# Optimization experiments

Hardware: AMD Instinct MI355X
Metric: run time of the kernel (lower is better)

## Reference

```python
import jax, jax.numpy as jnp
import numpy as np

N_HEAD = 16
HEAD_DIM = 64
ROPE_BASE = 10000.0


def _rope(t):
    # t: [B, H, C, D]; rotate-half RoPE, offset 0
    B, H, C, D = t.shape
    inv_freq = 1.0 / (ROPE_BASE ** (jnp.arange(0, D, 2, dtype=jnp.float32) / D))  # [D/2]
    ang = jnp.arange(C, dtype=jnp.float32)[:, None] * inv_freq[None, :]           # [C, D/2]
    cos = jnp.concatenate([jnp.cos(ang), jnp.cos(ang)], axis=-1)                  # [C, D]
    sin = jnp.concatenate([jnp.sin(ang), jnp.sin(ang)], axis=-1)                  # [C, D]
    t1, t2 = jnp.split(t, 2, axis=-1)
    rot = jnp.concatenate([-t2, t1], axis=-1)
    return t * cos.astype(t.dtype) + rot * sin.astype(t.dtype)


def setup_inputs() -> dict:
    key = jax.random.key(0)
    ks = jax.random.split(key, 5)
    E = 1024
    B, C = 2, 2048
    s = 1.0 / np.sqrt(E)
    return {
        "x": jax.random.normal(ks[0], (B, C, E), dtype=jnp.float32),
        "Wq": jax.random.normal(ks[1], (E, E), dtype=jnp.float32) * s,
        "Wk": jax.random.normal(ks[2], (E, E), dtype=jnp.float32) * s,
        "Wv": jax.random.normal(ks[3], (E, E), dtype=jnp.float32) * s,
        "Wo": jax.random.normal(ks[4], (E, E), dtype=jnp.float32) * s,
    }


def reference(x, Wq, Wk, Wv, Wo):
    B, C, E = x.shape
    H, D = N_HEAD, HEAD_DIM
    # nn.Linear(bias=False): y = x @ W.T
    Q = (x @ Wq.T).reshape(B, C, H, D).transpose(0, 2, 1, 3)  # [B,H,C,D]
    K = (x @ Wk.T).reshape(B, C, H, D).transpose(0, 2, 1, 3)
    V = (x @ Wv.T).reshape(B, C, H, D).transpose(0, 2, 1, 3)
    Q = _rope(Q)
    K = _rope(K)
    scores = jnp.einsum("bhqd,bhkd->bhqk", Q, K) / jnp.sqrt(jnp.float32(D))
    causal = jnp.tril(jnp.ones((C, C), dtype=bool))
    scores = jnp.where(causal, scores, jnp.float32(-jnp.inf))
    weights = jax.nn.softmax(scores, axis=-1)
    hidden = jnp.einsum("bhqk,bhkd->bhqd", weights, V)
    hidden = hidden.transpose(0, 2, 1, 3).reshape(B, C, H * D)
    return hidden @ Wo.T
```

## Files before the change

### kernel.cpp

```cpp
#include <hip/hip_runtime.h>
#include <hip/hip_bf16.h>

typedef __attribute__((ext_vector_type(8))) short bf16x8;
typedef __attribute__((ext_vector_type(4))) float f32x4;
typedef unsigned short u16;
typedef unsigned int u32;

#define SM_SCALE 0.18033688f


__device__ __forceinline__ u16 f2bf(float f) {
  __hip_bfloat16 h = __float2bfloat16(f);
  return *reinterpret_cast<u16*>(&h);
}

__device__ __forceinline__ void async16(const void* g, void* l) {
  __builtin_amdgcn_global_load_lds((const __attribute__((address_space(1))) u32*)g,
                                   (__attribute__((address_space(3))) u32*)l, 16, 0, 0);
}


__global__ void cast_bf16(const float4* __restrict__ src, ushort4* __restrict__ dst, int n4) {
  int stride = gridDim.x * blockDim.x;
  for (int i = blockIdx.x * blockDim.x + threadIdx.x; i < n4; i += stride) {
    float4 v = src[i];
    ushort4 o;
    o.x = f2bf(v.x); o.y = f2bf(v.y); o.z = f2bf(v.z); o.w = f2bf(v.w);
    dst[i] = o;
  }
}

__global__ void cast_w4(const float4* __restrict__ w0, const float4* __restrict__ w1,
                        const float4* __restrict__ w2, const float4* __restrict__ w3,
                        ushort4* __restrict__ o0, ushort4* __restrict__ o1,
                        ushort4* __restrict__ o2, ushort4* __restrict__ o3, int n4) {
  const float4* src = (blockIdx.y == 0) ? w0 : (blockIdx.y == 1) ? w1 : (blockIdx.y == 2) ? w2 : w3;
  ushort4* dst = (blockIdx.y == 0) ? o0 : (blockIdx.y == 1) ? o1 : (blockIdx.y == 2) ? o2 : o3;
  int stride = gridDim.x * blockDim.x;
  for (int i = blockIdx.x * blockDim.x + threadIdx.x; i < n4; i += stride) {
    float4 v = src[i];
    ushort4 o;
    o.x = f2bf(v.x); o.y = f2bf(v.y); o.z = f2bf(v.z); o.w = f2bf(v.w);
    dst[i] = o;
  }
}


__global__ void rope_table(float* __restrict__ tcos, float* __restrict__ tsin) {
  int idx = blockIdx.x * blockDim.x + threadIdx.x;
  if (idx >= 2048 * 32) return;
  int c = idx >> 5, j = idx & 31;
  float inv = powf(10000.f, -(float)j * (1.f / 32.f));
  float ang = (float)c * inv;
  tcos[idx] = cosf(ang);
  tsin[idx] = sinf(ang);
}


__launch_bounds__(256)
__global__ void qkv_gemm(const u16* __restrict__ xb, const u16* __restrict__ Wqb,
                         const u16* __restrict__ Wkb, const u16* __restrict__ Wvb,
                         const float* __restrict__ tcos, const float* __restrict__ tsin,
                         u16* __restrict__ Qr, u16* __restrict__ Kr, u16* __restrict__ Vt) {
  const int z = blockIdx.z;
  const u16* W = (z == 0) ? Wqb : (z == 1) ? Wkb : Wvb;
  u16* dst = (z == 0) ? Qr : (z == 1) ? Kr : Vt;
  const int m0 = blockIdx.y * 128, n0 = blockIdx.x * 128;
  const int tid = threadIdx.x, w = tid >> 6, lane = tid & 63, g = lane >> 4, cl = lane & 15;
  const int wr = w >> 1, wc = w & 1;
  __shared__ u16 As[128][32], Bs[128][32];
  f32x4 acc[4][4] = {};
  for (int k0 = 0; k0 < 1024; k0 += 32) {
#pragma unroll
    for (int ch = 0; ch < 2; ++ch) {
      int t = tid + ch * 256;
      int row = t >> 2, col = (t & 3) * 8;
      async16(&xb[(size_t)(m0 + row) * 1024 + k0 + col], &As[row][col]);
      async16(&W[(size_t)(n0 + row) * 1024 + k0 + col], &Bs[row][col]);
    }
    __syncthreads();
    bf16x8 af[4], bfr[4];
#pragma unroll
    for (int i = 0; i < 4; ++i) af[i] = *(const bf16x8*)&As[wr * 64 + i * 16 + cl][g * 8];
#pragma unroll
    for (int j = 0; j < 4; ++j) bfr[j] = *(const bf16x8*)&Bs[wc * 64 + j * 16 + cl][g * 8];
#pragma unroll
    for (int i = 0; i < 4; ++i)
#pragma unroll
      for (int j = 0; j < 4; ++j)
        acc[i][j] = __builtin_amdgcn_mfma_f32_16x16x32_bf16(af[i], bfr[j], acc[i][j], 0, 0, 0);
    __syncthreads();
  }
  if (z < 2) {
#pragma unroll
    for (int i = 0; i < 4; ++i) {
      int mbase = m0 + wr * 64 + i * 16 + g * 4;
#pragma unroll
      for (int r = 0; r < 4; ++r) {
        int mm = mbase + r;
        int b = mm >> 11, pos = mm & 2047;
#pragma unroll
        for (int j = 0; j < 2; ++j) {
          int n = n0 + wc * 64 + j * 16 + cl;
          int h = n >> 6, dlo = n & 63;
          float a = acc[i][j][r], b2 = acc[i][j + 2][r];
          float cv = tcos[pos * 32 + dlo], sv = tsin[pos * 32 + dlo];
          float o1 = a * cv - b2 * sv;
          float o2 = b2 * cv + a * sv;
          size_t base = ((size_t)(b * 16 + h) * 2048 + pos) * 64;
          dst[base + dlo] = f2bf(o1);
          dst[base + dlo + 32] = f2bf(o2);
        }
      }
    }
  } else {
#pragma unroll
    for (int i = 0; i < 4; ++i) {
      int mbase = m0 + wr * 64 + i * 16 + g * 4;
      int b = mbase >> 11, pos = mbase & 2047;
#pragma unroll
      for (int j = 0; j < 4; ++j) {
        int n = n0 + wc * 64 + j * 16 + cl;
        int h = n >> 6, d = n & 63;
        ushort4 v4;
        v4.x = f2bf(acc[i][j][0]);
        v4.y = f2bf(acc[i][j][1]);
        v4.z = f2bf(acc[i][j][2]);
        v4.w = f2bf(acc[i][j][3]);
        *(ushort4*)&dst[((size_t)(b * 16 + h) * 64 + d) * 2048 + pos] = v4;
      }
    }
  }
}


__launch_bounds__(64)
__global__ void attn_kernel(const u16* __restrict__ Qr, const u16* __restrict__ Kr,
                            const u16* __restrict__ Vt, u16* __restrict__ hid) {
  const int bid = blockIdx.x;
  const int xcd = bid & 7, c = (bid >> 3) & 31, slot = bid >> 8;
  const int bh = xcd * 4 + (slot >> 1);
  const int qt = (slot & 1) ? c : 63 - c;
  const int lane = threadIdx.x, g = lane >> 4, cl = lane & 15;
  const int b = bh >> 4, h = bh & 15;
  const int qbase = qt * 32;
  const u16* Qp = Qr + (size_t)bh * 2048 * 64;
  const u16* Kp = Kr + (size_t)bh * 2048 * 64;
  const u16* Vp = Vt + (size_t)bh * 2048 * 64;
  __shared__ u16 Pt[32 * 64];

  bf16x8 aq[4];
#pragma unroll
  for (int qg = 0; qg < 2; ++qg)
#pragma unroll
    for (int ks = 0; ks < 2; ++ks)
      aq[qg * 2 + ks] = *(const bf16x8*)&Qp[(size_t)(qbase + qg * 16 + cl) * 64 + ks * 32 + g * 8];

  f32x4 ot[8] = {};
  float mrow[2], lrow[2];
  mrow[0] = mrow[1] = -__builtin_inff();
  lrow[0] = lrow[1] = 0.f;

  const int ktmax = qt >> 1;

  auto loadK = [&](bf16x8* dst, int kt_) {
#pragma unroll
    for (int n = 0; n < 4; ++n)
#pragma unroll
      for (int ks = 0; ks < 2; ++ks)
        dst[n * 2 + ks] = *(const bf16x8*)&Kp[(size_t)(kt_ * 64 + n * 16 + cl) * 64 + ks * 32 + g * 8];
  };
  auto loadV = [&](bf16x8* dst, int kt_) {
#pragma unroll
    for (int ks = 0; ks < 2; ++ks)
#pragma unroll
      for (int j = 0; j < 4; ++j)
        dst[ks * 4 + j] = *(const bf16x8*)&Vp[(size_t)(j * 16 + cl) * 2048 + kt_ * 64 + ks * 32 + g * 8];
  };

  auto tile = [&](const bf16x8* kf, const bf16x8* bv, int kt_, bool diag) {
    f32x4 st[8] = {};
#pragma unroll
    for (int qg = 0; qg < 2; ++qg)
#pragma unroll
      for (int n = 0; n < 4; ++n)
#pragma unroll
        for (int ks = 0; ks < 2; ++ks)
          st[qg * 4 + n] = __builtin_amdgcn_mfma_f32_16x16x32_bf16(kf[n * 2 + ks], aq[qg * 2 + ks],
                                                                   st[qg * 4 + n], 0, 0, 0);
    if (diag) {
#pragma unroll
      for (int qg = 0; qg < 2; ++qg) {
        int q = qbase + qg * 16 + cl;
#pragma unroll
        for (int n = 0; n < 4; ++n)
#pragma unroll
          for (int r = 0; r < 4; ++r) {
            int k = kt_ * 64 + n * 16 + g * 4 + r;
            st[qg * 4 + n][r] = (k <= q) ? st[qg * 4 + n][r] * SM_SCALE : -__builtin_inff();
          }
      }
    } else {
#pragma unroll
      for (int i = 0; i < 8; ++i)
#pragma unroll
        for (int r = 0; r < 4; ++r) st[i][r] *= SM_SCALE;
    }
    bf16x8 ap[4];
#pragma unroll
    for (int qg = 0; qg < 2; ++qg) {
      float v0 = fmaxf(fmaxf(st[qg * 4 + 0][0], st[qg * 4 + 0][1]),
                       fmaxf(st[qg * 4 + 0][2], st[qg * 4 + 0][3]));
      float v1 = fmaxf(fmaxf(st[qg * 4 + 1][0], st[qg * 4 + 1][1]),
                       fmaxf(st[qg * 4 + 1][2], st[qg * 4 + 1][3]));
      float v2 = fmaxf(fmaxf(st[qg * 4 + 2][0], st[qg * 4 + 2][1]),
                       fmaxf(st[qg * 4 + 2][2], st[qg * 4 + 2][3]));
      float v3 = fmaxf(fmaxf(st[qg * 4 + 3][0], st[qg * 4 + 3][1]),
                       fmaxf(st[qg * 4 + 3][2], st[qg * 4 + 3][3]));
      float v = fmaxf(fmaxf(v0, v1), fmaxf(v2, v3));
      v = fmaxf(v, __shfl_xor(v, 16));
      v = fmaxf(v, __shfl_xor(v, 32));
      float mnew = fmaxf(mrow[qg], v);
      float ef = exp2f(mrow[qg] - mnew);
      mrow[qg] = mnew;
      float rs = 0.f;
      int rowq = qg * 16 + cl;
#pragma unroll
      for (int n = 0; n < 4; ++n) {
        float p0 = exp2f(st[qg * 4 + n][0] - mnew);
        float p1 = exp2f(st[qg * 4 + n][1] - mnew);
        float p2 = exp2f(st[qg * 4 + n][2] - mnew);
        float p3 = exp2f(st[qg * 4 + n][3] - mnew);
        rs += (p0 + p1) + (p2 + p3);
        ushort4 v4;
        v4.x = f2bf(p0); v4.y = f2bf(p1); v4.z = f2bf(p2); v4.w = f2bf(p3);
        *(ushort4*)&Pt[(rowq * 64 + n * 16 + g * 4) ^ ((rowq & 7) << 3)] = v4;
      }
      rs += __shfl_xor(rs, 16);
      rs += __shfl_xor(rs, 32);
      lrow[qg] = lrow[qg] * ef + rs;
#pragma unroll
      for (int j = 0; j < 4; ++j)
#pragma unroll
        for (int r = 0; r < 4; ++r) ot[qg * 4 + j][r] *= ef;
#pragma unroll
      for (int ks = 0; ks < 2; ++ks)
        ap[qg * 2 + ks] = *(const bf16x8*)&Pt[(rowq * 64 + ks * 32 + g * 8) ^ ((rowq & 7) << 3)];
    }
#pragma unroll
    for (int qg = 0; qg < 2; ++qg)
#pragma unroll
      for (int ks = 0; ks < 2; ++ks)
#pragma unroll
        for (int j = 0; j < 4; ++j)
          ot[qg * 4 + j] = __builtin_amdgcn_mfma_f32_16x16x32_bf16(bv[ks * 4 + j], ap[qg * 2 + ks],
                                                                   ot[qg * 4 + j], 0, 0, 0);
  };

  bf16x8 kA[8], kB[8], bv[8];
  loadK(kA, 0);
  for (int kt = 0; kt <= ktmax; kt += 2) {
    loadV(bv, kt);
    if (kt + 1 <= ktmax) loadK(kB, kt + 1);
    tile(kA, bv, kt, kt == ktmax);
    if (kt + 1 <= ktmax) {
      loadV(bv, kt + 1);
      if (kt + 2 <= ktmax) loadK(kA, kt + 2);
      tile(kB, bv, kt + 1, kt + 1 == ktmax);
    }
  }

#pragma unroll
  for (int qg = 0; qg < 2; ++qg) {
    float inv = 1.f / lrow[qg];
    int q = qbase + qg * 16 + cl;
#pragma unroll
    for (int j = 0; j < 4; ++j) {
      ushort4 v4;
      v4.x = f2bf(ot[qg * 4 + j][0] * inv);
      v4.y = f2bf(ot[qg * 4 + j][1] * inv);
      v4.z = f2bf(ot[qg * 4 + j][2] * inv);
      v4.w = f2bf(ot[qg * 4 + j][3] * inv);
      *(ushort4*)&hid[((size_t)(b * 2048) + q) * 1024 + h * 64 + j * 16 + g * 4] = v4;
    }
  }
}


__launch_bounds__(256)
__global__ void out_gemm(const u16* __restrict__ hb, const u16* __restrict__ Wob,
                         float* __restrict__ out) {
  const int m0 = blockIdx.y * 128, n0 = blockIdx.x * 128;
  const int tid = threadIdx.x, w = tid >> 6, lane = tid & 63, g = lane >> 4, cl = lane & 15;
  const int wr = w >> 1, wc = w & 1;
  __shared__ u16 As[128][32], Bs[128][32];
  f32x4 acc[4][4] = {};
  for (int k0 = 0; k0 < 1024; k0 += 32) {
#pragma unroll
    for (int ch = 0; ch < 2; ++ch) {
      int t = tid + ch * 256;
      int row = t >> 2, col = (t & 3) * 8;
      async16(&hb[(size_t)(m0 + row) * 1024 + k0 + col], &As[row][col]);
      async16(&Wob[(size_t)(n0 + row) * 1024 + k0 + col], &Bs[row][col]);
    }
    __syncthreads();
    bf16x8 af[4], bfr[4];
#pragma unroll
    for (int i = 0; i < 4; ++i) af[i] = *(const bf16x8*)&As[wr * 64 + i * 16 + cl][g * 8];
#pragma unroll
    for (int j = 0; j < 4; ++j) bfr[j] = *(const bf16x8*)&Bs[wc * 64 + j * 16 + cl][g * 8];
#pragma unroll
    for (int i = 0; i < 4; ++i)
#pragma unroll
      for (int j = 0; j < 4; ++j)
        acc[i][j] = __builtin_amdgcn_mfma_f32_16x16x32_bf16(af[i], bfr[j], acc[i][j], 0, 0, 0);
    __syncthreads();
  }
#pragma unroll
  for (int i = 0; i < 4; ++i)
#pragma unroll
    for (int r = 0; r < 4; ++r) {
      int m = m0 + wr * 64 + i * 16 + g * 4 + r;
#pragma unroll
      for (int j = 0; j < 4; ++j)
        out[(size_t)m * 1024 + n0 + wc * 64 + j * 16 + cl] = acc[i][j][r];
    }
}


extern "C" void kernel_launch(void* const* d_in, const int* in_sizes, int n_in,
                              void* d_out, int out_size, void* d_ws, size_t ws_size,
                              hipStream_t stream) {
  const float* x = (const float*)d_in[0];
  const float* Wq = (const float*)d_in[1];
  const float* Wk = (const float*)d_in[2];
  const float* Wv = (const float*)d_in[3];
  const float* Wo = (const float*)d_in[4];
  float* out = (float*)d_out;

  char* ws = (char*)d_ws;
  size_t off = 0;
  auto alloc = [&](size_t bytes) {
    void* p = ws + off;
    off += (bytes + 255) & ~(size_t)255;
    return p;
  };
  u16* xb = (u16*)alloc(4096ull * 1024 * 2);
  u16* Wqb = (u16*)alloc(1024ull * 1024 * 2);
  u16* Wkb = (u16*)alloc(1024ull * 1024 * 2);
  u16* Wvb = (u16*)alloc(1024ull * 1024 * 2);
  u16* Wob = (u16*)alloc(1024ull * 1024 * 2);
  u16* Qr = (u16*)alloc(4096ull * 1024 * 2);
  u16* Kr = (u16*)alloc(4096ull * 1024 * 2);
  u16* Vt = (u16*)alloc(4096ull * 1024 * 2);
  u16* hid = (u16*)alloc(4096ull * 1024 * 2);
  float* tcos = (float*)alloc(2048ull * 32 * 4);
  float* tsin = (float*)alloc(2048ull * 32 * 4);

  cast_bf16<<<1024, 256, 0, stream>>>((const float4*)x, (ushort4*)xb, 4096 * 1024 / 4);
  cast_w4<<<dim3(256, 4), 256, 0, stream>>>((const float4*)Wq, (const float4*)Wk,
                                            (const float4*)Wv, (const float4*)Wo,
                                            (ushort4*)Wqb, (ushort4*)Wkb,
                                            (ushort4*)Wvb, (ushort4*)Wob, 1024 * 1024 / 4);
  rope_table<<<256, 256, 0, stream>>>(tcos, tsin);

  qkv_gemm<<<dim3(8, 32, 3), 256, 0, stream>>>(xb, Wqb, Wkb, Wvb, tcos, tsin, Qr, Kr, Vt);
  attn_kernel<<<2048, 64, 0, stream>>>(Qr, Kr, Vt, hid);
  out_gemm<<<dim3(8, 32), 256, 0, stream>>>(hid, Wob, out);
}
```

Baseline: 243.9 us.

## Process two 16-row query tiles per wave with mirrored causal pairing

The attention kernel shrinks each query tile from 32 to 16 rows. Each block now loops over two tiles, p and 127-p, so causal work is balanced within a block instead of across blocks. This halves the per-tile register and LDS footprint and evens out per-block work. In exchange, each K/V tile loaded serves only 16 query rows, so global K/V traffic and MFMA B-operand reuse get worse.

```diff
diff --git a/kernel.cpp b/kernel.cpp
--- a/kernel.cpp
+++ b/kernel.cpp
@@ -140,28 +140,13 @@
   const int bid = blockIdx.x;
   const int xcd = bid & 7, c = (bid >> 3) & 31, slot = bid >> 8;
   const int bh = xcd * 4 + (slot >> 1);
-  const int qt = (slot & 1) ? c : 63 - c;
+  const int p = c | ((slot & 1) << 5);
   const int lane = threadIdx.x, g = lane >> 4, cl = lane & 15;
   const int b = bh >> 4, h = bh & 15;
-  const int qbase = qt * 32;
   const u16* Qp = Qr + (size_t)bh * 2048 * 64;
   const u16* Kp = Kr + (size_t)bh * 2048 * 64;
   const u16* Vp = Vt + (size_t)bh * 2048 * 64;
-  __shared__ u16 Pt[32 * 64];
-
-  bf16x8 aq[4];
-#pragma unroll
-  for (int qg = 0; qg < 2; ++qg)
-#pragma unroll
-    for (int ks = 0; ks < 2; ++ks)
-      aq[qg * 2 + ks] = *(const bf16x8*)&Qp[(size_t)(qbase + qg * 16 + cl) * 64 + ks * 32 + g * 8];
-
-  f32x4 ot[8] = {};
-  float mrow[2], lrow[2];
-  mrow[0] = mrow[1] = -__builtin_inff();
-  lrow[0] = lrow[1] = 0.f;
-
-  const int ktmax = qt >> 1;
+  __shared__ u16 Pt[16 * 64];
 
   auto loadK = [&](bf16x8* dst, int kt_) {
 #pragma unroll
@@ -178,109 +163,104 @@
         dst[ks * 4 + j] = *(const bf16x8*)&Vp[(size_t)(j * 16 + cl) * 2048 + kt_ * 64 + ks * 32 + g * 8];
   };
 
-  auto tile = [&](const bf16x8* kf, const bf16x8* bv, int kt_, bool diag) {
-    f32x4 st[8] = {};
-#pragma unroll
-    for (int qg = 0; qg < 2; ++qg)
+#pragma unroll 1
+  for (int qi = 0; qi < 2; ++qi) {
+    const int qt = qi ? p : 127 - p;
+    const int qbase = qt * 16;
+    const int ktmax = qt >> 2;
+
+    bf16x8 aq[2];
+#pragma unroll
+    for (int ks = 0; ks < 2; ++ks)
+      aq[ks] = *(const bf16x8*)&Qp[(size_t)(qbase + cl) * 64 + ks * 32 + g * 8];
+
+    f32x4 ot[4] = {};
+    float mrow = -__builtin_inff(), lrow = 0.f;
+
+    auto tile = [&](const bf16x8* kf, const bf16x8* bv, int kt_, bool diag) {
+      f32x4 st[4] = {};
 #pragma unroll
       for (int n = 0; n < 4; ++n)
 #pragma unroll
         for (int ks = 0; ks < 2; ++ks)
-          st[qg * 4 + n] = __builtin_amdgcn_mfma_f32_16x16x32_bf16(kf[n * 2 + ks], aq[qg * 2 + ks],
-                                                                   st[qg * 4 + n], 0, 0, 0);
-    if (diag) {
-#pragma unroll
-      for (int qg = 0; qg < 2; ++qg) {
-        int q = qbase + qg * 16 + cl;
+          st[n] = __builtin_amdgcn_mfma_f32_16x16x32_bf16(kf[n * 2 + ks], aq[ks], st[n], 0, 0, 0);
+      if (diag) {
+        int q = qbase + cl;
 #pragma unroll
         for (int n = 0; n < 4; ++n)
 #pragma unroll
           for (int r = 0; r < 4; ++r) {
             int k = kt_ * 64 + n * 16 + g * 4 + r;
-            st[qg * 4 + n][r] = (k <= q) ? st[qg * 4 + n][r] * SM_SCALE : -__builtin_inff();
+            st[n][r] = (k <= q) ? st[n][r] * SM_SCALE : -__builtin_inff();
           }
-      }
-    } else {
-#pragma unroll
-      for (int i = 0; i < 8; ++i)
-#pragma unroll
-        for (int r = 0; r < 4; ++r) st[i][r] *= SM_SCALE;
-    }
-    bf16x8 ap[4];
-#pragma unroll
-    for (int qg = 0; qg < 2; ++qg) {
-      float v0 = fmaxf(fmaxf(st[qg * 4 + 0][0], st[qg * 4 + 0][1]),
-                       fmaxf(st[qg * 4 + 0][2], st[qg * 4 + 0][3]));
-      float v1 = fmaxf(fmaxf(st[qg * 4 + 1][0], st[qg * 4 + 1][1]),
-                       fmaxf(st[qg * 4 + 1][2], st[qg * 4 + 1][3]));
-      float v2 = fmaxf(fmaxf(st[qg * 4 + 2][0], st[qg * 4 + 2][1]),
-                       fmaxf(st[qg * 4 + 2][2], st[qg * 4 + 2][3]));
-      float v3 = fmaxf(fmaxf(st[qg * 4 + 3][0], st[qg * 4 + 3][1]),
-                       fmaxf(st[qg * 4 + 3][2], st[qg * 4 + 3][3]));
+      } else {
+#pragma unroll
+        for (int n = 0; n < 4; ++n)
+#pragma unroll
+          for (int r = 0; r < 4; ++r) st[n][r] *= SM_SCALE;
+      }
+      float v0 = fmaxf(fmaxf(st[0][0], st[0][1]), fmaxf(st[0][2], st[0][3]));
+      float v1 = fmaxf(fmaxf(st[1][0], st[1][1]), fmaxf(st[1][2], st[1][3]));
+      float v2 = fmaxf(fmaxf(st[2][0], st[2][1]), fmaxf(st[2][2], st[2][3]));
+      float v3 = fmaxf(fmaxf(st[3][0], st[3][1]), fmaxf(st[3][2], st[3][3]));
       float v = fmaxf(fmaxf(v0, v1), fmaxf(v2, v3));
       v = fmaxf(v, __shfl_xor(v, 16));
       v = fmaxf(v, __shfl_xor(v, 32));
-      float mnew = fmaxf(mrow[qg], v);
-      float ef = exp2f(mrow[qg] - mnew);
-      mrow[qg] = mnew;
+      float mnew = fmaxf(mrow, v);
+      float ef = exp2f(mrow - mnew);
+      mrow = mnew;
       float rs = 0.f;
-      int rowq = qg * 16 + cl;
 #pragma unroll
       for (int n = 0; n < 4; ++n) {
-        float p0 = exp2f(st[qg * 4 + n][0] - mnew);
-        float p1 = exp2f(st[qg * 4 + n][1] - mnew);
-        float p2 = exp2f(st[qg * 4 + n][2] - mnew);
-        float p3 = exp2f(st[qg * 4 + n][3] - mnew);
+        float p0 = exp2f(st[n][0] - mnew);
+        float p1 = exp2f(st[n][1] - mnew);
+        float p2 = exp2f(st[n][2] - mnew);
+        float p3 = exp2f(st[n][3] - mnew);
         rs += (p0 + p1) + (p2 + p3);
         ushort4 v4;
         v4.x = f2bf(p0); v4.y = f2bf(p1); v4.z = f2bf(p2); v4.w = f2bf(p3);
-        *(ushort4*)&Pt[(rowq * 64 + n * 16 + g * 4) ^ ((rowq & 7) << 3)] = v4;
+        *(ushort4*)&Pt[(cl * 64 + n * 16 + g * 4) ^ ((cl & 7) << 3)] = v4;
       }
       rs += __shfl_xor(rs, 16);
       rs += __shfl_xor(rs, 32);
-      lrow[qg] = lrow[qg] * ef + rs;
-#pragma unroll
-      for (int j = 0; j < 4; ++j)
-#pragma unroll
-        for (int r = 0; r < 4; ++r) ot[qg * 4 + j][r] *= ef;
+      lrow = lrow * ef + rs;
+#pragma unroll
+      for (int j = 0; j < 4; ++j)
+#pragma unroll
+        for (int r = 0; r < 4; ++r) ot[j][r] *= ef;
+      bf16x8 ap[2];
 #pragma unroll
       for (int ks = 0; ks < 2; ++ks)
-        ap[qg * 2 + ks] = *(const bf16x8*)&Pt[(rowq * 64 + ks * 32 + g * 8) ^ ((rowq & 7) << 3)];
-    }
-#pragma unroll
-    for (int qg = 0; qg < 2; ++qg)
+        ap[ks] = *(const bf16x8*)&Pt[(cl * 64 + ks * 32 + g * 8) ^ ((cl & 7) << 3)];
 #pragma unroll
       for (int ks = 0; ks < 2; ++ks)
 #pragma unroll
         for (int j = 0; j < 4; ++j)
-          ot[qg * 4 + j] = __builtin_amdgcn_mfma_f32_16x16x32_bf16(bv[ks * 4 + j], ap[qg * 2 + ks],
-                                                                   ot[qg * 4 + j], 0, 0, 0);
-  };
-
-  bf16x8 kA[8], kB[8], bv[8];
-  loadK(kA, 0);
-  for (int kt = 0; kt <= ktmax; kt += 2) {
-    loadV(bv, kt);
-    if (kt + 1 <= ktmax) loadK(kB, kt + 1);
-    tile(kA, bv, kt, kt == ktmax);
-    if (kt + 1 <= ktmax) {
-      loadV(bv, kt + 1);
-      if (kt + 2 <= ktmax) loadK(kA, kt + 2);
-      tile(kB, bv, kt + 1, kt + 1 == ktmax);
-    }
-  }
-
-#pragma unroll
-  for (int qg = 0; qg < 2; ++qg) {
-    float inv = 1.f / lrow[qg];
-    int q = qbase + qg * 16 + cl;
+          ot[j] = __builtin_amdgcn_mfma_f32_16x16x32_bf16(bv[ks * 4 + j], ap[ks], ot[j], 0, 0, 0);
+    };
+
+    bf16x8 kA[8], kB[8], bv[8];
+    loadK(kA, 0);
+    for (int kt = 0; kt <= ktmax; kt += 2) {
+      loadV(bv, kt);
+      if (kt + 1 <= ktmax) loadK(kB, kt + 1);
+      tile(kA, bv, kt, kt == ktmax);
+      if (kt + 1 <= ktmax) {
+        loadV(bv, kt + 1);
+        if (kt + 2 <= ktmax) loadK(kA, kt + 2);
+        tile(kB, bv, kt + 1, kt + 1 == ktmax);
+      }
+    }
+
+    float inv = 1.f / lrow;
+    int q = qbase + cl;
 #pragma unroll
     for (int j = 0; j < 4; ++j) {
       ushort4 v4;
-      v4.x = f2bf(ot[qg * 4 + j][0] * inv);
-      v4.y = f2bf(ot[qg * 4 + j][1] * inv);
-      v4.z = f2bf(ot[qg * 4 + j][2] * inv);
-      v4.w = f2bf(ot[qg * 4 + j][3] * inv);
+      v4.x = f2bf(ot[j][0] * inv);
+      v4.y = f2bf(ot[j][1] * inv);
+      v4.z = f2bf(ot[j][2] * inv);
+      v4.w = f2bf(ot[j][3] * inv);
       *(ushort4*)&hid[((size_t)(b * 2048) + q) * 1024 + h * 64 + j * 16 + g * 4] = v4;
     }
   }
```

Measured after the change: 277.7 us. +13.8%, slower.
